# Kernel tuning notes

Hardware: AMD Instinct MI355X
Metric: run time of the kernel (lower is better)

Reference implementation:

```python
import jax, jax.numpy as jnp
import numpy as np

B, S, DIM = 2, 2048, 1024
H, DH = 16, 64
WIN = 512


def setup_inputs() -> dict:
    key = jax.random.key(0)
    k1, k2, k3 = jax.random.split(key, 3)
    x = jax.random.normal(k1, (B, S, DIM), dtype=jnp.float32)
    Wqkv = jax.random.normal(k2, (DIM, 3 * H * DH), dtype=jnp.float32) * (DIM ** -0.5)
    Wout = jax.random.normal(k3, (H * DH, DIM), dtype=jnp.float32) * ((H * DH) ** -0.5)
    return {"x": x, "Wqkv": Wqkv, "Wout": Wout}


def reference(x, Wqkv, Wout):
    b, s, _ = x.shape
    qkv = jnp.einsum('bsd,de->bse', x, Wqkv)  # (B,S,3*H*DH)
    q, k, v = jnp.split(qkv, 3, axis=-1)
    # -> (B,H,S,DH)
    q = q.reshape(b, s, H, DH).transpose(0, 2, 1, 3)
    k = k.reshape(b, s, H, DH).transpose(0, 2, 1, 3)
    v = v.reshape(b, s, H, DH).transpose(0, 2, 1, 3)
    scale = DH ** -0.5  # attention sees per-head dim
    scores = jnp.einsum('bhsd,bhtd->bhst', q, k) * scale  # dense (B,H,S,S)
    i = jnp.arange(s)[:, None]
    j = jnp.arange(s)[None, :]
    mask = (j >= i - WIN + 1) & (j <= i)  # causal sliding window
    mask_value = -jnp.finfo(scores.dtype).max
    scores = jnp.where(mask[None, None], scores, mask_value)
    attn = jax.nn.softmax(scores, axis=-1)
    out = jnp.einsum('bhst,bhtd->bhsd', attn, v)
    out = out.transpose(0, 2, 1, 3).reshape(b, s, H * DH)
    return jnp.einsum('bse,ed->bsd', out, Wout)
```

## Files before the change

### kernel.cpp

```cpp
#include <hip/hip_runtime.h>

#define S_LEN 2048
#define BATCH 2
#define HDIM 1024
#define NH 16
#define DH 64
#define WINSZ 512
#define MROWS (BATCH * S_LEN)

typedef __attribute__((ext_vector_type(8))) short bfrag;
typedef __attribute__((ext_vector_type(4))) float f32x4;
typedef __attribute__((ext_vector_type(4))) int i128;

__device__ __forceinline__ short f2bf(float f) {
    union { float f; unsigned u; } v;
    v.f = f;
    unsigned r = v.u + 0x7fffu + ((v.u >> 16) & 1u);
    return (short)(r >> 16);
}

__device__ __forceinline__ void gload_lds16(const short* g, short* l) {
    __builtin_amdgcn_global_load_lds(
        (const __attribute__((address_space(1))) unsigned int*)g,
        (__attribute__((address_space(3))) unsigned int*)l, 16, 0, 0);
}

__global__ __launch_bounds__(256)
void prep_kernel(const float* __restrict__ x, const float* __restrict__ Wqkv,
                 const float* __restrict__ Wout,
                 short* __restrict__ x_bf, short* __restrict__ wqkv_t, short* __restrict__ wout_t)
{
    __shared__ float tile[32][33];
    const int bid = blockIdx.x;
    const int t = threadIdx.x;

    if (bid < 4096) {
        int i = bid * 256 + t;
        float4 v = ((const float4*)x)[i];
        union { short s[4]; int2 p; } u;
        u.s[0] = f2bf(v.x); u.s[1] = f2bf(v.y); u.s[2] = f2bf(v.z); u.s[3] = f2bf(v.w);
        ((int2*)x_bf)[i] = u.p;
        return;
    }

    const float* in;
    short* out;
    int R, C, bx, by;
    if (bid < 7168) {
        int lb = bid - 4096;
        in = Wqkv; out = wqkv_t; R = 1024; C = 3072;
        bx = lb % 96; by = lb / 96;
    } else {
        int lb = bid - 7168;
        in = Wout; out = wout_t; R = 1024; C = 1024;
        bx = lb & 31; by = lb >> 5;
    }
    int tc0 = bx * 32, tr0 = by * 32;
    int c = t & 31, r0 = t >> 5;
    #pragma unroll
    for (int k = 0; k < 4; ++k) {
        int r = r0 + k * 8;
        tile[r][c] = in[(size_t)(tr0 + r) * C + tc0 + c];
    }
    __syncthreads();
    int r2p = (t & 15) << 1, c0 = t >> 4;
    #pragma unroll
    for (int k = 0; k < 2; ++k) {
        int c2 = c0 + k * 16;
        union { short sh[2]; int w; } u;
        u.sh[0] = f2bf(tile[r2p][c2]);
        u.sh[1] = f2bf(tile[r2p + 1][c2]);
        *(int*)(&out[(size_t)(tc0 + c2) * R + tr0 + r2p]) = u.w;
    }
}

__global__ __launch_bounds__(256, 3)
void gemm_qkv(const short* __restrict__ A, const short* __restrict__ Bt,
              short* __restrict__ qk_rm, short* __restrict__ vto)
{
    __shared__ __align__(16) short smraw[17408];
    short (*Al)[4096] = (short(*)[4096])smraw;
    short (*Bl)[4096] = (short(*)[4096])(smraw + 8192);
    const int K = HDIM;
    const int t = threadIdx.x;
    const int lane = t & 63;
    const int wave = t >> 6;
    const int wr = wave >> 1, wc = wave & 1;
    const int m0 = blockIdx.y * 128, n0 = blockIdx.x * 128;
    const int lq = lane & 15;
    const int g = lane >> 4;
    const int lk8 = g << 3;

    f32x4 acc[4][4];
    #pragma unroll
    for (int m = 0; m < 4; ++m)
        #pragma unroll
        for (int n = 0; n < 4; ++n)
            acc[m][n] = (f32x4){0.f, 0.f, 0.f, 0.f};

    const int row0s = t >> 2, col0s = (t & 3) << 3;
    const int row1s = (256 + t) >> 2;
    const size_t dst0 = (size_t)(wave * 64) * 8;
    const size_t dst1 = (size_t)(256 + wave * 64) * 8;

    auto stage = [&](int k0, int sb) {
        gload_lds16(&A[(size_t)(m0 + row0s) * K + k0 + col0s], &Al[sb][0] + dst0);
        gload_lds16(&Bt[(size_t)(n0 + row0s) * K + k0 + col0s], &Bl[sb][0] + dst0);
        gload_lds16(&A[(size_t)(m0 + row1s) * K + k0 + col0s], &Al[sb][0] + dst1);
        gload_lds16(&Bt[(size_t)(n0 + row1s) * K + k0 + col0s], &Bl[sb][0] + dst1);
    };

    const int nk = K >> 5;
    stage(0, 0);
    __syncthreads();
    for (int ki = 0; ki < nk; ++ki) {
        const int cur = ki & 1;
        if (ki + 1 < nk) stage((ki + 1) << 5, cur ^ 1);
        bfrag af[4], bfr[4];
        #pragma unroll
        for (int m = 0; m < 4; ++m)
            af[m] = *(const bfrag*)(&Al[cur][(wr * 64 + m * 16 + lq) * 32 + lk8]);
        #pragma unroll
        for (int n = 0; n < 4; ++n)
            bfr[n] = *(const bfrag*)(&Bl[cur][(wc * 64 + n * 16 + lq) * 32 + lk8]);
        #pragma unroll
        for (int m = 0; m < 4; ++m)
            #pragma unroll
            for (int n = 0; n < 4; ++n)
                acc[m][n] = __builtin_amdgcn_mfma_f32_16x16x32_bf16(af[m], bfr[n], acc[m][n], 0, 0, 0);
        __syncthreads();
    }

    if (n0 < 2048) {
        #pragma unroll
        for (int m = 0; m < 4; ++m)
            #pragma unroll
            for (int n = 0; n < 4; ++n) {
                int col = n0 + wc * 64 + n * 16 + lq;
                int row0 = m0 + wr * 64 + m * 16 + g * 4;
                #pragma unroll
                for (int r = 0; r < 4; ++r)
                    qk_rm[(size_t)(row0 + r) * 2048 + col] = f2bf(acc[m][n][r]);
            }
    } else {
        short* T = smraw;
        #pragma unroll
        for (int m = 0; m < 4; ++m)
            #pragma unroll
            for (int n = 0; n < 4; ++n) {
                int cl = wc * 64 + n * 16 + lq;
                int rl0 = wr * 64 + m * 16 + g * 4;
                union { short sh[4]; int2 w; } u;
                #pragma unroll
                for (int r = 0; r < 4; ++r) u.sh[r] = f2bf(acc[m][n][r]);
                *(int2*)(&T[cl * 136 + rl0]) = u.w;
            }
        __syncthreads();
        const int b = m0 >> 11, sbase = m0 & 2047;
        const int h0 = (n0 - 2048) >> 6;
        #pragma unroll
        for (int i = 0; i < 8; ++i) {
            int c2 = i * 256 + t;
            int rv = c2 >> 4;
            int sc = (c2 & 15) << 3;
            int h = h0 + (rv >> 6), dh = rv & 63;
            i128 v = *(const i128*)(&T[rv * 136 + sc]);
            *(i128*)(&vto[((size_t)((b * NH + h) * DH + dh)) * S_LEN + sbase + sc]) = v;
        }
    }
}

__global__ __launch_bounds__(256, 2)
void gemm_out(const short* __restrict__ A, const short* __restrict__ Bt,
              float* __restrict__ co)
{
    __shared__ __align__(16) short Al[2][128 * 64];
    __shared__ __align__(16) short Bl[2][128 * 64];
    const int K = HDIM, N = HDIM;
    const int t = threadIdx.x;
    const int lane = t & 63;
    const int wave = t >> 6;
    const int wr = wave >> 1, wc = wave & 1;
    const int m0 = blockIdx.y * 128, n0 = blockIdx.x * 128;
    const int lq = lane & 15;
    const int g = lane >> 4;

    f32x4 acc[4][4];
    #pragma unroll
    for (int m = 0; m < 4; ++m)
        #pragma unroll
        for (int n = 0; n < 4; ++n)
            acc[m][n] = (f32x4){0.f, 0.f, 0.f, 0.f};

    auto stage = [&](int k0, int sb) {
        #pragma unroll
        for (int q = 0; q < 4; ++q) {
            int chunk = q * 256 + t;
            int row = chunk >> 3, col = (chunk & 7) << 3;
            size_t dst = (size_t)(q * 256 + wave * 64) * 8;
            gload_lds16(&A[(size_t)(m0 + row) * K + k0 + col], &Al[sb][0] + dst);
            gload_lds16(&Bt[(size_t)(n0 + row) * K + k0 + col], &Bl[sb][0] + dst);
        }
    };

    const int nk = K >> 6;
    stage(0, 0);
    __syncthreads();
    for (int ki = 0; ki < nk; ++ki) {
        const int cur = ki & 1;
        if (ki + 1 < nk) stage((ki + 1) << 6, cur ^ 1);
        bfrag af[4][2], bfr[4][2];
        #pragma unroll
        for (int m = 0; m < 4; ++m)
            #pragma unroll
            for (int ks = 0; ks < 2; ++ks)
                af[m][ks] = *(const bfrag*)(&Al[cur][(wr * 64 + m * 16 + lq) * 64 + ks * 32 + (g << 3)]);
        #pragma unroll
        for (int n = 0; n < 4; ++n)
            #pragma unroll
            for (int ks = 0; ks < 2; ++ks)
                bfr[n][ks] = *(const bfrag*)(&Bl[cur][(wc * 64 + n * 16 + lq) * 64 + ks * 32 + (g << 3)]);
        #pragma unroll
        for (int m = 0; m < 4; ++m)
            #pragma unroll
            for (int n = 0; n < 4; ++n) {
                acc[m][n] = __builtin_amdgcn_mfma_f32_16x16x32_bf16(af[m][0], bfr[n][0], acc[m][n], 0, 0, 0);
                acc[m][n] = __builtin_amdgcn_mfma_f32_16x16x32_bf16(af[m][1], bfr[n][1], acc[m][n], 0, 0, 0);
            }
        __syncthreads();
    }

    #pragma unroll
    for (int m = 0; m < 4; ++m)
        #pragma unroll
        for (int n = 0; n < 4; ++n) {
            int col = n0 + wc * 64 + n * 16 + lq;
            int row0 = m0 + wr * 64 + m * 16 + g * 4;
            #pragma unroll
            for (int r = 0; r < 4; ++r)
                co[(size_t)(row0 + r) * N + col] = acc[m][n][r];
        }
}

__global__ __launch_bounds__(256, 3)
void attn_kernel(const short* __restrict__ qk, const short* __restrict__ vt,
                 short* __restrict__ attno)
{
    __shared__ __align__(16) short Kl[2][64 * 64];
    __shared__ __align__(16) short Vl[2][64 * 64];
    __shared__ __align__(16) short Pl[4][32 * 64];

    const int bid = blockIdx.x;
    const int logical = (bid & 7) * 64 + (bid >> 3);
    const int qblk = logical & 15;
    const int bh = logical >> 4;
    const int b = bh >> 4, h = bh & 15;

    const int t = threadIdx.x;
    const int wave = t >> 6, lane = t & 63;
    const int qb0 = qblk * 128;
    const int i0 = qb0 + wave * 32;
    const short* qbase = qk + (size_t)b * S_LEN * 2048 + h * 64;
    const short* kbase = qk + (size_t)b * S_LEN * 2048 + 1024 + h * 64;
    const short* vp = vt + (size_t)bh * DH * S_LEN;
    char* myP = (char*)&Pl[wave][0];

    const int lq = lane & 15;
    const int g = lane >> 4;
    const int swz = (lq & 7) << 4;
    const int l7 = lq & 7;

    bfrag qf[2][2];
    #pragma unroll
    for (int qq = 0; qq < 2; ++qq) {
        qf[qq][0] = *(const bfrag*)(&qbase[(size_t)(i0 + qq * 16 + lq) * 2048 + (g << 3)]);
        qf[qq][1] = *(const bfrag*)(&qbase[(size_t)(i0 + qq * 16 + lq) * 2048 + 32 + (g << 3)]);
    }

    f32x4 oacc[2][4];
    #pragma unroll
    for (int qq = 0; qq < 2; ++qq)
        #pragma unroll
        for (int d = 0; d < 4; ++d) oacc[qq][d] = (f32x4){0.f, 0.f, 0.f, 0.f};
    float m2[2] = {-1e30f, -1e30f}, lrun[2] = {0.f, 0.f};
    const float QSCALE = 0.125f * 1.44269504f;

    int j_lo = qb0 - (WINSZ - 1);
    if (j_lo < 0) j_lo = 0;
    j_lo &= ~63;
    const int nT = ((qb0 + 128) - j_lo) >> 6;

    auto stage = [&](int jrel, short* kbuf, short* vbuf) {
        #pragma unroll
        for (int qq2 = 0; qq2 < 2; ++qq2) {
            int chunk = qq2 * 256 + wave * 64 + lane;
            int row = chunk >> 3;
            int cc = (chunk & 7) ^ (row & 7);
            short* kdst = kbuf + (size_t)(qq2 * 256 + wave * 64) * 8;
            short* vdst = vbuf + (size_t)(qq2 * 256 + wave * 64) * 8;
            gload_lds16(kbase + (size_t)(j_lo + jrel + row) * 2048 + cc * 8, kdst);
            gload_lds16(vp + (size_t)row * S_LEN + j_lo + jrel + cc * 8, vdst);
        }
    };

    stage(0, Kl[0], Vl[0]);
    __syncthreads();

    for (int ti = 0; ti < nT; ++ti) {
        const int cur = ti & 1;
        const int j0 = j_lo + ti * 64;
        if (ti + 1 < nT) stage((ti + 1) * 64, Kl[cur ^ 1], Vl[cur ^ 1]);

        const short* Kc = Kl[cur];
        const short* Vc = Vl[cur];

        #pragma unroll
        for (int qq = 0; qq < 2; ++qq) {
            const int i0q = i0 + qq * 16;
            const int qi = i0q + lq;

            f32x4 sc[4];
            __builtin_amdgcn_s_setprio(1);
            #pragma unroll
            for (int tc = 0; tc < 4; ++tc) {
                bfrag a0 = *(const bfrag*)(&Kc[(tc * 16 + lq) * 64 + ((g ^ l7) << 3)]);
                bfrag a1 = *(const bfrag*)(&Kc[(tc * 16 + lq) * 64 + (((4 | g) ^ l7) << 3)]);
                f32x4 z = (f32x4){0.f, 0.f, 0.f, 0.f};
                z = __builtin_amdgcn_mfma_f32_16x16x32_bf16(a0, qf[qq][0], z, 0, 0, 0);
                z = __builtin_amdgcn_mfma_f32_16x16x32_bf16(a1, qf[qq][1], z, 0, 0, 0);
                sc[tc] = z;
            }
            __builtin_amdgcn_s_setprio(0);

            const bool nomask = (j0 >= i0q - (WINSZ - 16)) && (j0 + 63 <= i0q);
            float s[4][4];
            float pm = -1e30f;
            #pragma unroll
            for (int tc = 0; tc < 4; ++tc)
                #pragma unroll
                for (int r = 0; r < 4; ++r) {
                    float sv = sc[tc][r] * QSCALE;
                    if (!nomask) {
                        int kj = j0 + tc * 16 + 4 * g + r;
                        sv = ((kj <= qi) && (kj > qi - WINSZ)) ? sv : -1e30f;
                    }
                    s[tc][r] = sv;
                    pm = fmaxf(pm, sv);
                }
            pm = fmaxf(pm, __shfl_xor(pm, 16));
            pm = fmaxf(pm, __shfl_xor(pm, 32));
            float mnew = fmaxf(m2[qq], pm);
            float scale_old = exp2f(m2[qq] - mnew);
            m2[qq] = mnew;
            float p[4][4];
            float rs = 0.f;
            #pragma unroll
            for (int tc = 0; tc < 4; ++tc)
                #pragma unroll
                for (int r = 0; r < 4; ++r) {
                    p[tc][r] = exp2f(s[tc][r] - mnew);
                    rs += p[tc][r];
                }
            rs += __shfl_xor(rs, 16);
            rs += __shfl_xor(rs, 32);
            lrun[qq] = lrun[qq] * scale_old + rs;
            #pragma unroll
            for (int d = 0; d < 4; ++d) {
                f32x4 o = oacc[qq][d];
                o[0] *= scale_old; o[1] *= scale_old; o[2] *= scale_old; o[3] *= scale_old;
                oacc[qq][d] = o;
            }

            char* myPq = myP + qq * 2048;
            #pragma unroll
            for (int tc = 0; tc < 4; ++tc) {
                union { short sh[4]; int2 w; } u;
                u.sh[0] = f2bf(p[tc][0]); u.sh[1] = f2bf(p[tc][1]);
                u.sh[2] = f2bf(p[tc][2]); u.sh[3] = f2bf(p[tc][3]);
                int wb = (lq * 128 + tc * 32 + g * 8) ^ swz;
                *(int2*)(myPq + wb) = u.w;
            }
            asm volatile("s_waitcnt lgkmcnt(0)" ::: "memory");

            __builtin_amdgcn_s_setprio(1);
            #pragma unroll
            for (int kt = 0; kt < 2; ++kt) {
                int rb = (lq * 128 + kt * 64 + g * 16) ^ swz;
                bfrag pf = *(const bfrag*)(myPq + rb);
                #pragma unroll
                for (int d = 0; d < 4; ++d) {
                    bfrag vfr = *(const bfrag*)(&Vc[(d * 16 + lq) * 64 + (((kt * 4 + g) ^ l7) << 3)]);
                    oacc[qq][d] = __builtin_amdgcn_mfma_f32_16x16x32_bf16(vfr, pf, oacc[qq][d], 0, 0, 0);
                }
            }
            __builtin_amdgcn_s_setprio(0);
        }
        __syncthreads();
    }

    #pragma unroll
    for (int qq = 0; qq < 2; ++qq) {
        const float inv_l = 1.f / lrun[qq];
        const int qi = i0 + qq * 16 + lq;
        size_t rowbase = ((size_t)(b * S_LEN + qi)) * HDIM + h * DH;
        #pragma unroll
        for (int d = 0; d < 4; ++d) {
            union { short sh[4]; int2 w; } u;
            #pragma unroll
            for (int r = 0; r < 4; ++r)
                u.sh[r] = f2bf(oacc[qq][d][r] * inv_l);
            *(int2*)(&attno[rowbase + d * 16 + 4 * g]) = u.w;
        }
    }
}

extern "C" void kernel_launch(void* const* d_in, const int* in_sizes, int n_in,
                              void* d_out, int out_size, void* d_ws, size_t ws_size,
                              hipStream_t stream) {
    const float* x = (const float*)d_in[0];
    const float* Wqkv = (const float*)d_in[1];
    const float* Wout = (const float*)d_in[2];
    float* out = (float*)d_out;
    char* ws = (char*)d_ws;

    short* x_bf   = (short*)(ws);
    short* wqkv_t = (short*)(ws + 8388608);
    short* wout_t = (short*)(ws + 14680064);
    short* qk_rm  = (short*)(ws + 16777216);
    short* v_t    = (short*)(ws + 33554432);
    short* attno  = x_bf;

    prep_kernel<<<8192, 256, 0, stream>>>(x, Wqkv, Wout, x_bf, wqkv_t, wout_t);
    gemm_qkv<<<dim3(24, 32), 256, 0, stream>>>(x_bf, wqkv_t, qk_rm, v_t);
    attn_kernel<<<dim3(BATCH * NH * (S_LEN / 128)), 256, 0, stream>>>(qk_rm, v_t, attno);
    gemm_out<<<dim3(8, 32), 256, 0, stream>>>(attno, wout_t, out);
}
```

Before: 175.8 us.

## Halve attention query tile and defer PV MFMA to overlap with next QK

Each attention block now covers 64 query rows instead of 128, with one 16-row tile per wave, and the grid doubles to 1024 blocks with launch bounds raised to 4 blocks per CU. The P·V product for a key tile is deferred into the next iteration: P and V fragments are held in registers and issued after the next tile's loads start, with a rescale applied before accumulating. The aim is more parallelism and better MFMA/softmax overlap. The cost is that each K/V tile is loaded and staged by twice as many blocks, and more fragments stay live in registers.

```diff
diff --git a/kernel.cpp b/kernel.cpp
--- a/kernel.cpp
+++ b/kernel.cpp
@@ -242,24 +242,24 @@
         }
 }
 
-__global__ __launch_bounds__(256, 3)
+__global__ __launch_bounds__(256, 4)
 void attn_kernel(const short* __restrict__ qk, const short* __restrict__ vt,
                  short* __restrict__ attno)
 {
     __shared__ __align__(16) short Kl[2][64 * 64];
     __shared__ __align__(16) short Vl[2][64 * 64];
-    __shared__ __align__(16) short Pl[4][32 * 64];
+    __shared__ __align__(16) short Pl[4][16 * 64];
 
     const int bid = blockIdx.x;
-    const int logical = (bid & 7) * 64 + (bid >> 3);
-    const int qblk = logical & 15;
-    const int bh = logical >> 4;
+    const int logical = (bid & 7) * 128 + (bid >> 3);
+    const int qblk = logical & 31;
+    const int bh = logical >> 5;
     const int b = bh >> 4, h = bh & 15;
 
     const int t = threadIdx.x;
     const int wave = t >> 6, lane = t & 63;
-    const int qb0 = qblk * 128;
-    const int i0 = qb0 + wave * 32;
+    const int qb0 = qblk * 64;
+    const int i0 = qb0 + wave * 16;
     const short* qbase = qk + (size_t)b * S_LEN * 2048 + h * 64;
     const short* kbase = qk + (size_t)b * S_LEN * 2048 + 1024 + h * 64;
     const short* vp = vt + (size_t)bh * DH * S_LEN;
@@ -269,35 +269,34 @@
     const int g = lane >> 4;
     const int swz = (lq & 7) << 4;
     const int l7 = lq & 7;
-
-    bfrag qf[2][2];
-    #pragma unroll
-    for (int qq = 0; qq < 2; ++qq) {
-        qf[qq][0] = *(const bfrag*)(&qbase[(size_t)(i0 + qq * 16 + lq) * 2048 + (g << 3)]);
-        qf[qq][1] = *(const bfrag*)(&qbase[(size_t)(i0 + qq * 16 + lq) * 2048 + 32 + (g << 3)]);
-    }
-
-    f32x4 oacc[2][4];
-    #pragma unroll
-    for (int qq = 0; qq < 2; ++qq)
-        #pragma unroll
-        for (int d = 0; d < 4; ++d) oacc[qq][d] = (f32x4){0.f, 0.f, 0.f, 0.f};
-    float m2[2] = {-1e30f, -1e30f}, lrun[2] = {0.f, 0.f};
+    const int qi = i0 + lq;
+
+    bfrag qf[2];
+    qf[0] = *(const bfrag*)(&qbase[(size_t)(i0 + lq) * 2048 + (g << 3)]);
+    qf[1] = *(const bfrag*)(&qbase[(size_t)(i0 + lq) * 2048 + 32 + (g << 3)]);
+
+    f32x4 oacc[4];
+    #pragma unroll
+    for (int d = 0; d < 4; ++d) oacc[d] = (f32x4){0.f, 0.f, 0.f, 0.f};
+    float m2 = -1e30f, lrun = 0.f, scale_prev = 1.f;
     const float QSCALE = 0.125f * 1.44269504f;
+
+    bfrag pf_prev[2];
+    bfrag vf_prev[2][4];
 
     int j_lo = qb0 - (WINSZ - 1);
     if (j_lo < 0) j_lo = 0;
     j_lo &= ~63;
-    const int nT = ((qb0 + 128) - j_lo) >> 6;
+    const int nT = ((qb0 + 64) - j_lo) >> 6;
 
     auto stage = [&](int jrel, short* kbuf, short* vbuf) {
         #pragma unroll
-        for (int qq2 = 0; qq2 < 2; ++qq2) {
-            int chunk = qq2 * 256 + wave * 64 + lane;
+        for (int qq = 0; qq < 2; ++qq) {
+            int chunk = qq * 256 + wave * 64 + lane;
             int row = chunk >> 3;
             int cc = (chunk & 7) ^ (row & 7);
-            short* kdst = kbuf + (size_t)(qq2 * 256 + wave * 64) * 8;
-            short* vdst = vbuf + (size_t)(qq2 * 256 + wave * 64) * 8;
+            short* kdst = kbuf + (size_t)(qq * 256 + wave * 64) * 8;
+            short* vdst = vbuf + (size_t)(qq * 256 + wave * 64) * 8;
             gload_lds16(kbase + (size_t)(j_lo + jrel + row) * 2048 + cc * 8, kdst);
             gload_lds16(vp + (size_t)row * S_LEN + j_lo + jrel + cc * 8, vdst);
         }
@@ -311,106 +310,112 @@
         const int j0 = j_lo + ti * 64;
         if (ti + 1 < nT) stage((ti + 1) * 64, Kl[cur ^ 1], Vl[cur ^ 1]);
 
+        if (ti > 0) {
+            #pragma unroll
+            for (int d = 0; d < 4; ++d) {
+                f32x4 o = oacc[d];
+                o[0] *= scale_prev; o[1] *= scale_prev; o[2] *= scale_prev; o[3] *= scale_prev;
+                oacc[d] = o;
+            }
+            __builtin_amdgcn_s_setprio(1);
+            #pragma unroll
+            for (int kt = 0; kt < 2; ++kt)
+                #pragma unroll
+                for (int d = 0; d < 4; ++d)
+                    oacc[d] = __builtin_amdgcn_mfma_f32_16x16x32_bf16(vf_prev[kt][d], pf_prev[kt], oacc[d], 0, 0, 0);
+            __builtin_amdgcn_s_setprio(0);
+        }
+
         const short* Kc = Kl[cur];
         const short* Vc = Vl[cur];
 
-        #pragma unroll
-        for (int qq = 0; qq < 2; ++qq) {
-            const int i0q = i0 + qq * 16;
-            const int qi = i0q + lq;
-
-            f32x4 sc[4];
-            __builtin_amdgcn_s_setprio(1);
-            #pragma unroll
-            for (int tc = 0; tc < 4; ++tc) {
-                bfrag a0 = *(const bfrag*)(&Kc[(tc * 16 + lq) * 64 + ((g ^ l7) << 3)]);
-                bfrag a1 = *(const bfrag*)(&Kc[(tc * 16 + lq) * 64 + (((4 | g) ^ l7) << 3)]);
-                f32x4 z = (f32x4){0.f, 0.f, 0.f, 0.f};
-                z = __builtin_amdgcn_mfma_f32_16x16x32_bf16(a0, qf[qq][0], z, 0, 0, 0);
-                z = __builtin_amdgcn_mfma_f32_16x16x32_bf16(a1, qf[qq][1], z, 0, 0, 0);
-                sc[tc] = z;
-            }
-            __builtin_amdgcn_s_setprio(0);
-
-            const bool nomask = (j0 >= i0q - (WINSZ - 16)) && (j0 + 63 <= i0q);
-            float s[4][4];
-            float pm = -1e30f;
-            #pragma unroll
-            for (int tc = 0; tc < 4; ++tc)
-                #pragma unroll
-                for (int r = 0; r < 4; ++r) {
-                    float sv = sc[tc][r] * QSCALE;
-                    if (!nomask) {
-                        int kj = j0 + tc * 16 + 4 * g + r;
-                        sv = ((kj <= qi) && (kj > qi - WINSZ)) ? sv : -1e30f;
-                    }
-                    s[tc][r] = sv;
-                    pm = fmaxf(pm, sv);
+        f32x4 sc[4];
+        __builtin_amdgcn_s_setprio(1);
+        #pragma unroll
+        for (int tc = 0; tc < 4; ++tc) {
+            bfrag a0 = *(const bfrag*)(&Kc[(tc * 16 + lq) * 64 + ((g ^ l7) << 3)]);
+            bfrag a1 = *(const bfrag*)(&Kc[(tc * 16 + lq) * 64 + (((4 | g) ^ l7) << 3)]);
+            f32x4 z = (f32x4){0.f, 0.f, 0.f, 0.f};
+            z = __builtin_amdgcn_mfma_f32_16x16x32_bf16(a0, qf[0], z, 0, 0, 0);
+            z = __builtin_amdgcn_mfma_f32_16x16x32_bf16(a1, qf[1], z, 0, 0, 0);
+            sc[tc] = z;
+        }
+        __builtin_amdgcn_s_setprio(0);
+
+        const bool nomask = (j0 >= i0 - (WINSZ - 16)) && (j0 + 63 <= i0);
+        float s[4][4];
+        float pm = -1e30f;
+        #pragma unroll
+        for (int tc = 0; tc < 4; ++tc)
+            #pragma unroll
+            for (int r = 0; r < 4; ++r) {
+                float sv = sc[tc][r] * QSCALE;
+                if (!nomask) {
+                    int kj = j0 + tc * 16 + 4 * g + r;
+                    sv = ((kj <= qi) && (kj > qi - WINSZ)) ? sv : -1e30f;
                 }
-            pm = fmaxf(pm, __shfl_xor(pm, 16));
-            pm = fmaxf(pm, __shfl_xor(pm, 32));
-            float mnew = fmaxf(m2[qq], pm);
-            float scale_old = exp2f(m2[qq] - mnew);
-            m2[qq] = mnew;
-            float p[4][4];
-            float rs = 0.f;
-            #pragma unroll
-            for (int tc = 0; tc < 4; ++tc)
-                #pragma unroll
-                for (int r = 0; r < 4; ++r) {
-                    p[tc][r] = exp2f(s[tc][r] - mnew);
-                    rs += p[tc][r];
-                }
-            rs += __shfl_xor(rs, 16);
-            rs += __shfl_xor(rs, 32);
-            lrun[qq] = lrun[qq] * scale_old + rs;
-            #pragma unroll
-            for (int d = 0; d < 4; ++d) {
-                f32x4 o = oacc[qq][d];
-                o[0] *= scale_old; o[1] *= scale_old; o[2] *= scale_old; o[3] *= scale_old;
-                oacc[qq][d] = o;
-            }
-
-            char* myPq = myP + qq * 2048;
-            #pragma unroll
-            for (int tc = 0; tc < 4; ++tc) {
-                union { short sh[4]; int2 w; } u;
-                u.sh[0] = f2bf(p[tc][0]); u.sh[1] = f2bf(p[tc][1]);
-                u.sh[2] = f2bf(p[tc][2]); u.sh[3] = f2bf(p[tc][3]);
-                int wb = (lq * 128 + tc * 32 + g * 8) ^ swz;
-                *(int2*)(myPq + wb) = u.w;
-            }
-            asm volatile("s_waitcnt lgkmcnt(0)" ::: "memory");
-
-            __builtin_amdgcn_s_setprio(1);
-            #pragma unroll
-            for (int kt = 0; kt < 2; ++kt) {
-                int rb = (lq * 128 + kt * 64 + g * 16) ^ swz;
-                bfrag pf = *(const bfrag*)(myPq + rb);
-                #pragma unroll
-                for (int d = 0; d < 4; ++d) {
-                    bfrag vfr = *(const bfrag*)(&Vc[(d * 16 + lq) * 64 + (((kt * 4 + g) ^ l7) << 3)]);
-                    oacc[qq][d] = __builtin_amdgcn_mfma_f32_16x16x32_bf16(vfr, pf, oacc[qq][d], 0, 0, 0);
-                }
-            }
-            __builtin_amdgcn_s_setprio(0);
+                s[tc][r] = sv;
+                pm = fmaxf(pm, sv);
+            }
+        pm = fmaxf(pm, __shfl_xor(pm, 16));
+        pm = fmaxf(pm, __shfl_xor(pm, 32));
+        float mnew = fmaxf(m2, pm);
+        float scale_i = exp2f(m2 - mnew);
+        m2 = mnew;
+        float p[4][4];
+        float rs = 0.f;
+        #pragma unroll
+        for (int tc = 0; tc < 4; ++tc)
+            #pragma unroll
+            for (int r = 0; r < 4; ++r) {
+                p[tc][r] = exp2f(s[tc][r] - mnew);
+                rs += p[tc][r];
+            }
+        rs += __shfl_xor(rs, 16);
+        rs += __shfl_xor(rs, 32);
+        lrun = lrun * scale_i + rs;
+        scale_prev = scale_i;
+
+        #pragma unroll
+        for (int tc = 0; tc < 4; ++tc) {
+            union { short sh[4]; int2 w; } u;
+            u.sh[0] = f2bf(p[tc][0]); u.sh[1] = f2bf(p[tc][1]);
+            u.sh[2] = f2bf(p[tc][2]); u.sh[3] = f2bf(p[tc][3]);
+            int wb = (lq * 128 + tc * 32 + g * 8) ^ swz;
+            *(int2*)(myP + wb) = u.w;
+        }
+        #pragma unroll
+        for (int kt = 0; kt < 2; ++kt) {
+            int rb = (lq * 128 + kt * 64 + g * 16) ^ swz;
+            pf_prev[kt] = *(const bfrag*)(myP + rb);
+            #pragma unroll
+            for (int d = 0; d < 4; ++d)
+                vf_prev[kt][d] = *(const bfrag*)(&Vc[(d * 16 + lq) * 64 + (((kt * 4 + g) ^ l7) << 3)]);
         }
         __syncthreads();
     }
 
     #pragma unroll
-    for (int qq = 0; qq < 2; ++qq) {
-        const float inv_l = 1.f / lrun[qq];
-        const int qi = i0 + qq * 16 + lq;
-        size_t rowbase = ((size_t)(b * S_LEN + qi)) * HDIM + h * DH;
-        #pragma unroll
-        for (int d = 0; d < 4; ++d) {
-            union { short sh[4]; int2 w; } u;
-            #pragma unroll
-            for (int r = 0; r < 4; ++r)
-                u.sh[r] = f2bf(oacc[qq][d][r] * inv_l);
-            *(int2*)(&attno[rowbase + d * 16 + 4 * g]) = u.w;
-        }
+    for (int d = 0; d < 4; ++d) {
+        f32x4 o = oacc[d];
+        o[0] *= scale_prev; o[1] *= scale_prev; o[2] *= scale_prev; o[3] *= scale_prev;
+        oacc[d] = o;
+    }
+    #pragma unroll
+    for (int kt = 0; kt < 2; ++kt)
+        #pragma unroll
+        for (int d = 0; d < 4; ++d)
+            oacc[d] = __builtin_amdgcn_mfma_f32_16x16x32_bf16(vf_prev[kt][d], pf_prev[kt], oacc[d], 0, 0, 0);
+
+    const float inv_l = 1.f / lrun;
+    size_t rowbase = ((size_t)(b * S_LEN + qi)) * HDIM + h * DH;
+    #pragma unroll
+    for (int d = 0; d < 4; ++d) {
+        union { short sh[4]; int2 w; } u;
+        #pragma unroll
+        for (int r = 0; r < 4; ++r)
+            u.sh[r] = f2bf(oacc[d][r] * inv_l);
+        *(int2*)(&attno[rowbase + d * 16 + 4 * g]) = u.w;
     }
 }
 
@@ -432,6 +437,6 @@
 
     prep_kernel<<<8192, 256, 0, stream>>>(x, Wqkv, Wout, x_bf, wqkv_t, wout_t);
     gemm_qkv<<<dim3(24, 32), 256, 0, stream>>>(x_bf, wqkv_t, qk_rm, v_t);
-    attn_kernel<<<dim3(BATCH * NH * (S_LEN / 128)), 256, 0, stream>>>(qk_rm, v_t, attno);
+    attn_kernel<<<dim3(BATCH * NH * (S_LEN / 64)), 256, 0, stream>>>(qk_rm, v_t, attno);
     gemm_out<<<dim3(8, 32), 256, 0, stream>>>(attno, wout_t, out);
 }
```

Result: faster. 169.4 us (-3.7%).
